# Kernel optimization log

Measured on AMD Instinct MI355X. Metric: run time of the kernel, lower is better.

Reference implementation:

```python
import jax, jax.numpy as jnp
import numpy as np

B, D, R = 4096, 1024, 256
DT = 0.01
DT_SCALE = 1.0

# Yoshida 4th-order coefficients
_W1 = 1.0 / (2.0 - 2.0 ** (1.0 / 3.0))
_W0 = -(2.0 ** (1.0 / 3.0)) / (2.0 - 2.0 ** (1.0 / 3.0))
C1 = _W1 / 2.0
C2 = (_W0 + _W1) / 2.0
C3 = C2
C4 = C1
D1 = _W1
D2 = _W0
D3 = _W1


def setup_inputs() -> dict:
    key = jax.random.key(0)
    k1, k2, k3, k4, k5 = jax.random.split(key, 5)
    x = jax.random.normal(k1, (B, D), dtype=jnp.float32)
    v = jax.random.normal(k2, (B, D), dtype=jnp.float32)
    force = jax.random.normal(k3, (B, D), dtype=jnp.float32)
    # low-rank christoffel factors, scaled for numerical stability
    U = jax.random.normal(k4, (R, D), dtype=jnp.float32) * (1.0 / np.sqrt(D))
    W = jax.random.normal(k5, (D, R), dtype=jnp.float32) * (1.0 / np.sqrt(R))
    return {"x": x, "v": v, "force": force, "U": U, "W": W}


def _christoffel(tv, tx, U, W):
    # Gamma(v) = W @ (U v)^2  (low-rank quadratic form; x unused, matching
    # the gfn yoshida_fused(U, W) signature)
    h = jnp.einsum("rd,bd->br", U, tv)  # [B, R]
    return jnp.einsum("dr,br->bd", W, h * h)  # [B, D]


def reference(x, v, force, U, W):
    dt = DT * DT_SCALE

    def acceleration(tx, tv):
        return -_christoffel(tv, tx, U, W) + force

    x1 = x + C1 * dt * v
    v1 = v + D1 * dt * acceleration(x1, v)
    x2 = x1 + C2 * dt * v1
    v2 = v1 + D2 * dt * acceleration(x2, v1)
    x3 = x2 + C3 * dt * v2
    v3 = v2 + D3 * dt * acceleration(x3, v2)
    x_final = x3 + C4 * dt * v3
    return (x_final, v3)
```

## Files before the change

kernel.cpp:

```cpp
#include <hip/hip_runtime.h>


#define BSZ 4096
#define DD 1024
#define RR 256

#define U_OFF 0u
#define W_OFF (512u * 1024u)
#define M_OFF (1024u * 1024u)

typedef unsigned char uchar;
typedef unsigned int uint;
typedef unsigned short ushort;
typedef __attribute__((ext_vector_type(4))) float f32x4;
typedef __attribute__((ext_vector_type(4))) uint uint4v;
typedef __attribute__((ext_vector_type(8))) short short8;

__device__ inline uint f2bf1(float x) {
    uint u = __builtin_bit_cast(uint, x);
    return (u + 0x7FFFu + ((u >> 16) & 1u)) >> 16;
}
__device__ inline uint f2bf2(float lo, float hi) {
    return f2bf1(lo) | (f2bf1(hi) << 16);
}
__device__ inline uint cvt2(float a, float b) {
    const __bf16 lo = (__bf16)a, hi = (__bf16)b;
    return (uint)__builtin_bit_cast(ushort, lo) |
           ((uint)__builtin_bit_cast(ushort, hi) << 16);
}
__device__ inline uint4v frag8(const float4 a, const float4 b) {
    uint4v o;
    o.x = cvt2(a.x, a.y); o.y = cvt2(a.z, a.w);
    o.z = cvt2(b.x, b.y); o.w = cvt2(b.z, b.w);
    return o;
}

__global__ __launch_bounds__(256) void prep_kernel(
    const float* __restrict__ U, const float* __restrict__ W,
    uchar* __restrict__ ws)
{
    if (blockIdx.x < 192) {
        const int g = blockIdx.x * 256 + threadIdx.x;
        const int l = g & 63;
        const float* src;
        size_t dst;
        if (g < 32768) {
            const int slice = g >> 6, nt = slice >> 5, p = slice & 31;
            src = U + (size_t)(nt * 16 + (l & 15)) * DD + p * 32 + (l >> 4) * 8;
            dst = U_OFF + (size_t)slice * 1024 + l * 16;
        } else {
            const int g2 = g - 32768;
            const int slice = g2 >> 6, dt_ = slice >> 3, p = slice & 7;
            src = W + (size_t)(dt_ * 16 + (l & 15)) * RR + p * 32 + (l >> 4) * 8;
            dst = W_OFF + (size_t)slice * 1024 + l * 16;
        }
        const float4 a0 = *reinterpret_cast<const float4*>(src);
        const float4 a1 = *reinterpret_cast<const float4*>(src + 4);
        uint4v o;
        o.x = f2bf2(a0.x, a0.y); o.y = f2bf2(a0.z, a0.w);
        o.z = f2bf2(a1.x, a1.y); o.w = f2bf2(a1.z, a1.w);
        *reinterpret_cast<uint4v*>(ws + dst) = o;
    } else {
        const int bid = blockIdx.x - 192;
        const int rt = bid >> 4, ct = bid & 15;
        const int r = rt * 16 + (threadIdx.x >> 4);
        const int c = ct * 16 + (threadIdx.x & 15);
        const float* ur = U + (size_t)r * DD;
        const float* wc = W + c;
        float acc[8];
        #pragma unroll
        for (int i = 0; i < 8; ++i) acc[i] = 0.f;
        #pragma unroll 4
        for (int k = 0; k < DD; k += 8) {
            const float4 u0 = *reinterpret_cast<const float4*>(ur + k);
            const float4 u1 = *reinterpret_cast<const float4*>(ur + k + 4);
            acc[0] += u0.x * wc[(size_t)(k + 0) * RR];
            acc[1] += u0.y * wc[(size_t)(k + 1) * RR];
            acc[2] += u0.z * wc[(size_t)(k + 2) * RR];
            acc[3] += u0.w * wc[(size_t)(k + 3) * RR];
            acc[4] += u1.x * wc[(size_t)(k + 4) * RR];
            acc[5] += u1.y * wc[(size_t)(k + 5) * RR];
            acc[6] += u1.z * wc[(size_t)(k + 6) * RR];
            acc[7] += u1.w * wc[(size_t)(k + 7) * RR];
        }
        const float s = ((acc[0] + acc[1]) + (acc[2] + acc[3]))
                      + ((acc[4] + acc[5]) + (acc[6] + acc[7]));
        const int slice = ((r >> 4) << 3) + (c >> 5);
        const int ll = (r & 15) | (((c >> 3) & 3) << 4);
        *reinterpret_cast<ushort*>(
            ws + M_OFF + (size_t)slice * 1024 + ll * 16 + (c & 7) * 2)
            = (ushort)f2bf1(s);
    }
}

__global__ __launch_bounds__(1024) void yoshida_fused_kernel(
    const float* __restrict__ x_in,
    const float* __restrict__ v_in,
    const float* __restrict__ force,
    const uchar* __restrict__ ws,
    float* __restrict__ x_out,
    float* __restrict__ v_out)
{
    __shared__ __align__(16) uchar vA[32768];
    __shared__ __align__(16) uchar fA[32768];
    __shared__ __align__(16) uchar H2B0[8192];
    __shared__ __align__(16) uchar H2B1[8192];
    __shared__ __align__(16) uchar PB[8192];
    __shared__ __align__(16) uchar QB[8192];

    const int tid = threadIdx.x;
    const int w = tid >> 6, l = tid & 63;
    const int m = l & 15, q = l >> 4;
    const int b0 = blockIdx.x * 16;

    constexpr double CBRT2 = 1.2599210498948731647672106072782;
    constexpr double W1c = 1.0 / (2.0 - CBRT2);
    constexpr double W0c = -CBRT2 * W1c;
    constexpr double DTd = 0.01;
    constexpr double D1 = W1c, D2 = W0c, D3 = W1c;
    constexpr double C2c = (W0c + W1c) * 0.5, C4c = W1c * 0.5;
    constexpr double E1 = (C2c + C2c + C4c) * D1;
    constexpr double E2 = (C2c + C4c) * D2;
    constexpr double E3 = C4c * D3;
    const float dtf = (float)DTd, dt2 = (float)(DTd * DTd);
    const float se = (float)(E1 + E2 + E3);

    #pragma unroll
    for (int j = 0; j < 2; ++j) {
        const int p = 2 * w + j;
        const size_t so = (size_t)(b0 + m) * DD + p * 32 + q * 8;
        const float4 v0_ = *reinterpret_cast<const float4*>(v_in + so);
        const float4 v1_ = *reinterpret_cast<const float4*>(v_in + so + 4);
        const float4 f0_ = *reinterpret_cast<const float4*>(force + so);
        const float4 f1_ = *reinterpret_cast<const float4*>(force + so + 4);
        *reinterpret_cast<uint4v*>(vA + (size_t)p * 1024 + l * 16) = frag8(v0_, v1_);
        *reinterpret_cast<uint4v*>(fA + (size_t)p * 1024 + l * 16) = frag8(f0_, f1_);
    }

    const uchar* const up = ws + U_OFF + ((size_t)(w * 32) << 10) + l * 16;
    uint4v ub[8];
    #pragma unroll
    for (int p = 0; p < 8; ++p)
        ub[p] = *reinterpret_cast<const uint4v*>(up + ((size_t)p << 10));

    __syncthreads();

    f32x4 h = {0.f, 0.f, 0.f, 0.f}, g = {0.f, 0.f, 0.f, 0.f};
    #pragma unroll
    for (int p = 0; p < 32; ++p) {
        const uint4v uc = ub[p & 7];
        if (p < 24)
            ub[p & 7] = *reinterpret_cast<const uint4v*>(up + ((size_t)(p + 8) << 10));
        const short8 ua = __builtin_bit_cast(short8, uc);
        const short8 va = __builtin_bit_cast(short8,
            *reinterpret_cast<const uint4v*>(vA + ((size_t)p << 10) + l * 16));
        const short8 fa = __builtin_bit_cast(short8,
            *reinterpret_cast<const uint4v*>(fA + ((size_t)p << 10) + l * 16));
        h = __builtin_amdgcn_mfma_f32_16x16x32_bf16(ua, va, h, 0, 0, 0);
        g = __builtin_amdgcn_mfma_f32_16x16x32_bf16(ua, fa, g, 0, 0, 0);
    }

    const uchar* const mp = ws + M_OFF + ((size_t)(w * 8) << 10) + l * 16;
    uint4v mb[8];
    #pragma unroll
    for (int p = 0; p < 8; ++p)
        mb[p] = *reinterpret_cast<const uint4v*>(mp + ((size_t)p << 10));

    const int k0 = 16 * w + 4 * q;
    const int p0 = k0 >> 5;
    const int lp = ((k0 & 31) >> 3) * 16 + m;
    const int j0 = k0 & 7;
    const int hoff = p0 * 1024 + lp * 16 + j0 * 2;

    f32x4 P, Q;
    {
        float h2[4];
        #pragma unroll
        for (int i = 0; i < 4; ++i) h2[i] = h[i] * h[i];
        #pragma unroll
        for (int i = 0; i < 4; ++i) {
            P[i] = (float)D1 * h2[i];
            Q[i] = (float)E1 * h2[i];
        }
        *reinterpret_cast<uint*>(H2B0 + hoff)     = f2bf2(h2[0], h2[1]);
        *reinterpret_cast<uint*>(H2B0 + hoff + 4) = f2bf2(h2[2], h2[3]);
    }

    __syncthreads();
    {
        f32x4 acc = {0.f, 0.f, 0.f, 0.f};
        #pragma unroll
        for (int p = 0; p < 8; ++p) {
            const short8 hb = __builtin_bit_cast(short8,
                *reinterpret_cast<const uint4v*>(H2B0 + ((size_t)p << 10) + l * 16));
            acc = __builtin_amdgcn_mfma_f32_16x16x32_bf16(
                      __builtin_bit_cast(short8, mb[p]), hb, acc, 0, 0, 0);
        }
        const float cg = (float)(DTd * D1);
        #pragma unroll
        for (int i = 0; i < 4; ++i) h[i] += cg * (g[i] - acc[i]);
    }
    {
        float h2[4];
        #pragma unroll
        for (int i = 0; i < 4; ++i) h2[i] = h[i] * h[i];
        #pragma unroll
        for (int i = 0; i < 4; ++i) {
            P[i] += (float)D2 * h2[i];
            Q[i] += (float)E2 * h2[i];
        }
        *reinterpret_cast<uint*>(H2B1 + hoff)     = f2bf2(h2[0], h2[1]);
        *reinterpret_cast<uint*>(H2B1 + hoff + 4) = f2bf2(h2[2], h2[3]);
    }
    __syncthreads();
    {
        f32x4 acc = {0.f, 0.f, 0.f, 0.f};
        #pragma unroll
        for (int p = 0; p < 8; ++p) {
            const short8 hb = __builtin_bit_cast(short8,
                *reinterpret_cast<const uint4v*>(H2B1 + ((size_t)p << 10) + l * 16));
            acc = __builtin_amdgcn_mfma_f32_16x16x32_bf16(
                      __builtin_bit_cast(short8, mb[p]), hb, acc, 0, 0, 0);
        }
        const float cg = (float)(DTd * D2);
        #pragma unroll
        for (int i = 0; i < 4; ++i) h[i] += cg * (g[i] - acc[i]);
    }
    {
        float h2[4];
        #pragma unroll
        for (int i = 0; i < 4; ++i) h2[i] = h[i] * h[i];
        #pragma unroll
        for (int i = 0; i < 4; ++i) {
            P[i] += (float)D3 * h2[i];
            Q[i] += (float)E3 * h2[i];
        }
    }
    *reinterpret_cast<uint*>(PB + hoff)     = f2bf2(P[0], P[1]);
    *reinterpret_cast<uint*>(PB + hoff + 4) = f2bf2(P[2], P[3]);
    *reinterpret_cast<uint*>(QB + hoff)     = f2bf2(Q[0], Q[1]);
    *reinterpret_cast<uint*>(QB + hoff + 4) = f2bf2(Q[2], Q[3]);

    const uchar* const wpb = ws + W_OFF + l * 16;
    uint4v wb[4][2];
    #pragma unroll
    for (int p = 0; p < 4; ++p) {
        wb[p][0] = *reinterpret_cast<const uint4v*>(wpb + (size_t)((4 * w)     * 8 + p) * 1024);
        wb[p][1] = *reinterpret_cast<const uint4v*>(wpb + (size_t)((4 * w + 1) * 8 + p) * 1024);
    }

    __syncthreads();

    #pragma unroll
    for (int half = 0; half < 2; ++half) {
        const int t0 = 4 * w + half * 2;
        f32x4 aV[2] = {{0.f,0.f,0.f,0.f}, {0.f,0.f,0.f,0.f}};
        f32x4 aX[2] = {{0.f,0.f,0.f,0.f}, {0.f,0.f,0.f,0.f}};
        #pragma unroll
        for (int p = 0; p < 8; ++p) {
            const uint4v c0 = wb[p & 3][0];
            const uint4v c1 = wb[p & 3][1];
            if (p < 4) {
                wb[p & 3][0] = *reinterpret_cast<const uint4v*>(
                    wpb + (size_t)((t0)     * 8 + p + 4) * 1024);
                wb[p & 3][1] = *reinterpret_cast<const uint4v*>(
                    wpb + (size_t)((t0 + 1) * 8 + p + 4) * 1024);
            } else if (half == 0) {
                wb[p & 3][0] = *reinterpret_cast<const uint4v*>(
                    wpb + (size_t)((t0 + 2) * 8 + (p - 4)) * 1024);
                wb[p & 3][1] = *reinterpret_cast<const uint4v*>(
                    wpb + (size_t)((t0 + 3) * 8 + (p - 4)) * 1024);
            }
            const short8 pb = __builtin_bit_cast(short8,
                *reinterpret_cast<const uint4v*>(PB + ((size_t)p << 10) + l * 16));
            const short8 qb = __builtin_bit_cast(short8,
                *reinterpret_cast<const uint4v*>(QB + ((size_t)p << 10) + l * 16));
            const short8 w0 = __builtin_bit_cast(short8, c0);
            const short8 w1 = __builtin_bit_cast(short8, c1);
            aV[0] = __builtin_amdgcn_mfma_f32_16x16x32_bf16(w0, pb, aV[0], 0, 0, 0);
            aV[1] = __builtin_amdgcn_mfma_f32_16x16x32_bf16(w1, pb, aV[1], 0, 0, 0);
            aX[0] = __builtin_amdgcn_mfma_f32_16x16x32_bf16(w0, qb, aX[0], 0, 0, 0);
            aX[1] = __builtin_amdgcn_mfma_f32_16x16x32_bf16(w1, qb, aX[1], 0, 0, 0);
        }
        #pragma unroll
        for (int t = 0; t < 2; ++t) {
            const size_t gib = (size_t)(b0 + m) * DD + (t0 + t) * 16 + 4 * q;
            const float4 fv = *reinterpret_cast<const float4*>(force + gib);
            const float4 v0 = *reinterpret_cast<const float4*>(v_in + gib);
            const float4 x0 = *reinterpret_cast<const float4*>(x_in + gib);
            float4 vo, xo;
            vo.x = v0.x + dtf * fv.x - dtf * aV[t][0];
            vo.y = v0.y + dtf * fv.y - dtf * aV[t][1];
            vo.z = v0.z + dtf * fv.z - dtf * aV[t][2];
            vo.w = v0.w + dtf * fv.w - dtf * aV[t][3];
            xo.x = x0.x + dtf * v0.x + dt2 * se * fv.x - dt2 * aX[t][0];
            xo.y = x0.y + dtf * v0.y + dt2 * se * fv.y - dt2 * aX[t][1];
            xo.z = x0.z + dtf * v0.z + dt2 * se * fv.z - dt2 * aX[t][2];
            xo.w = x0.w + dtf * v0.w + dt2 * se * fv.w - dt2 * aX[t][3];
            *reinterpret_cast<float4*>(v_out + gib) = vo;
            *reinterpret_cast<float4*>(x_out + gib) = xo;
        }
    }
}

extern "C" void kernel_launch(void* const* d_in, const int* in_sizes, int n_in,
                              void* d_out, int out_size, void* d_ws, size_t ws_size,
                              hipStream_t stream) {
    const float* x     = (const float*)d_in[0];
    const float* v     = (const float*)d_in[1];
    const float* force = (const float*)d_in[2];
    const float* U     = (const float*)d_in[3];
    const float* W     = (const float*)d_in[4];

    float* x_out = (float*)d_out;
    float* v_out = x_out + (size_t)BSZ * DD;

    uchar* ws = (uchar*)d_ws;

    prep_kernel<<<dim3(448), dim3(256), 0, stream>>>(U, W, ws);
    yoshida_fused_kernel<<<dim3(BSZ / 16), dim3(1024), 0, stream>>>(
        x, v, force, ws, x_out, v_out);
}
```

Measured before the change: 148.0 us.

## Split fused integrator into H/G projection kernel and D-split iteration kernel

Breaks the single fused kernel into a separate kernel that computes the U projections of v and force, storing them as fp32 in workspace, and an iteration kernel launched with twice as many blocks, each covering half of D for the output GEMM. The UW product is now computed with MFMA in its own kernel instead of scalar FMAs. The aim is more parallelism and less serial work per block. The cost is two extra launches and an HBM round-trip for the H/G intermediates, and the redundant Christoffel iterations now run in both halves.

```diff
diff --git a/kernel.cpp b/kernel.cpp
--- a/kernel.cpp
+++ b/kernel.cpp
@@ -8,6 +8,8 @@
 #define U_OFF 0u
 #define W_OFF (512u * 1024u)
 #define M_OFF (1024u * 1024u)
+#define H_OFF (2u * 1024u * 1024u)
+#define G_OFF (6u * 1024u * 1024u)
 
 typedef unsigned char uchar;
 typedef unsigned int uint;
@@ -35,74 +37,142 @@
     return o;
 }
 
-__global__ __launch_bounds__(256) void prep_kernel(
+__global__ __launch_bounds__(256) void pack_kernel(
     const float* __restrict__ U, const float* __restrict__ W,
     uchar* __restrict__ ws)
 {
-    if (blockIdx.x < 192) {
-        const int g = blockIdx.x * 256 + threadIdx.x;
-        const int l = g & 63;
-        const float* src;
-        size_t dst;
-        if (g < 32768) {
-            const int slice = g >> 6, nt = slice >> 5, p = slice & 31;
-            src = U + (size_t)(nt * 16 + (l & 15)) * DD + p * 32 + (l >> 4) * 8;
-            dst = U_OFF + (size_t)slice * 1024 + l * 16;
-        } else {
-            const int g2 = g - 32768;
-            const int slice = g2 >> 6, dt_ = slice >> 3, p = slice & 7;
-            src = W + (size_t)(dt_ * 16 + (l & 15)) * RR + p * 32 + (l >> 4) * 8;
-            dst = W_OFF + (size_t)slice * 1024 + l * 16;
-        }
-        const float4 a0 = *reinterpret_cast<const float4*>(src);
-        const float4 a1 = *reinterpret_cast<const float4*>(src + 4);
-        uint4v o;
-        o.x = f2bf2(a0.x, a0.y); o.y = f2bf2(a0.z, a0.w);
-        o.z = f2bf2(a1.x, a1.y); o.w = f2bf2(a1.z, a1.w);
-        *reinterpret_cast<uint4v*>(ws + dst) = o;
+    const int g = blockIdx.x * 256 + threadIdx.x;
+    const int l = g & 63;
+    const float* src;
+    size_t dst;
+    if (g < 32768) {
+        const int slice = g >> 6, nt = slice >> 5, p = slice & 31;
+        src = U + (size_t)(nt * 16 + (l & 15)) * DD + p * 32 + (l >> 4) * 8;
+        dst = U_OFF + (size_t)slice * 1024 + l * 16;
     } else {
-        const int bid = blockIdx.x - 192;
-        const int rt = bid >> 4, ct = bid & 15;
-        const int r = rt * 16 + (threadIdx.x >> 4);
-        const int c = ct * 16 + (threadIdx.x & 15);
-        const float* ur = U + (size_t)r * DD;
-        const float* wc = W + c;
-        float acc[8];
-        #pragma unroll
-        for (int i = 0; i < 8; ++i) acc[i] = 0.f;
-        #pragma unroll 4
-        for (int k = 0; k < DD; k += 8) {
-            const float4 u0 = *reinterpret_cast<const float4*>(ur + k);
-            const float4 u1 = *reinterpret_cast<const float4*>(ur + k + 4);
-            acc[0] += u0.x * wc[(size_t)(k + 0) * RR];
-            acc[1] += u0.y * wc[(size_t)(k + 1) * RR];
-            acc[2] += u0.z * wc[(size_t)(k + 2) * RR];
-            acc[3] += u0.w * wc[(size_t)(k + 3) * RR];
-            acc[4] += u1.x * wc[(size_t)(k + 4) * RR];
-            acc[5] += u1.y * wc[(size_t)(k + 5) * RR];
-            acc[6] += u1.z * wc[(size_t)(k + 6) * RR];
-            acc[7] += u1.w * wc[(size_t)(k + 7) * RR];
-        }
-        const float s = ((acc[0] + acc[1]) + (acc[2] + acc[3]))
-                      + ((acc[4] + acc[5]) + (acc[6] + acc[7]));
+        const int g2 = g - 32768;
+        const int slice = g2 >> 6, dt_ = slice >> 3, p = slice & 7;
+        src = W + (size_t)(dt_ * 16 + (l & 15)) * RR + p * 32 + (l >> 4) * 8;
+        dst = W_OFF + (size_t)slice * 1024 + l * 16;
+    }
+    const float4 a0 = *reinterpret_cast<const float4*>(src);
+    const float4 a1 = *reinterpret_cast<const float4*>(src + 4);
+    uint4v o;
+    o.x = f2bf2(a0.x, a0.y); o.y = f2bf2(a0.z, a0.w);
+    o.z = f2bf2(a1.x, a1.y); o.w = f2bf2(a1.z, a1.w);
+    *reinterpret_cast<uint4v*>(ws + dst) = o;
+}
+
+__global__ __launch_bounds__(256) void mm_kernel(
+    const float* __restrict__ W, uchar* __restrict__ ws)
+{
+    const int tid = threadIdx.x;
+    const int wv = tid >> 6, l = tid & 63;
+    const int m_ = l & 15, q = l >> 4;
+    const int task = blockIdx.x * 4 + wv;
+    const int rt = task >> 4, ct = task & 15;
+
+    const uchar* ua_base = ws + U_OFF + ((size_t)(rt * 32) << 10) + l * 16;
+    const float* wc = W + ct * 16 + m_;
+
+    f32x4 acc = {0.f, 0.f, 0.f, 0.f};
+    #pragma unroll 8
+    for (int p = 0; p < 32; ++p) {
+        const uint4v ua = *reinterpret_cast<const uint4v*>(ua_base + ((size_t)p << 10));
+        const int dbase = p * 32 + q * 8;
+        float w8[8];
+        #pragma unroll
+        for (int j = 0; j < 8; ++j) w8[j] = wc[(size_t)(dbase + j) * RR];
+        uint4v bb;
+        bb.x = cvt2(w8[0], w8[1]); bb.y = cvt2(w8[2], w8[3]);
+        bb.z = cvt2(w8[4], w8[5]); bb.w = cvt2(w8[6], w8[7]);
+        acc = __builtin_amdgcn_mfma_f32_16x16x32_bf16(
+                  __builtin_bit_cast(short8, ua),
+                  __builtin_bit_cast(short8, bb), acc, 0, 0, 0);
+    }
+    #pragma unroll
+    for (int i = 0; i < 4; ++i) {
+        const int r = rt * 16 + 4 * q + i;
+        const int c = ct * 16 + m_;
         const int slice = ((r >> 4) << 3) + (c >> 5);
         const int ll = (r & 15) | (((c >> 3) & 3) << 4);
         *reinterpret_cast<ushort*>(
             ws + M_OFF + (size_t)slice * 1024 + ll * 16 + (c & 7) * 2)
-            = (ushort)f2bf1(s);
-    }
-}
-
-__global__ __launch_bounds__(1024) void yoshida_fused_kernel(
+            = (ushort)f2bf1(acc[i]);
+    }
+}
+
+__global__ __launch_bounds__(512) void hg_kernel(
+    const float* __restrict__ v_in, const float* __restrict__ force,
+    const uchar* __restrict__ ws, float* __restrict__ Hf, float* __restrict__ Gf)
+{
+    __shared__ __align__(16) uchar vA[32768];
+    __shared__ __align__(16) uchar fA[32768];
+
+    const int tid = threadIdx.x;
+    const int w = tid >> 6, l = tid & 63;
+    const int m = l & 15, q = l >> 4;
+    const int b0 = blockIdx.x * 16;
+
+    #pragma unroll
+    for (int j = 0; j < 4; ++j) {
+        const int p = 4 * w + j;
+        const size_t so = (size_t)(b0 + m) * DD + p * 32 + q * 8;
+        const float4 v0 = *reinterpret_cast<const float4*>(v_in + so);
+        const float4 v1 = *reinterpret_cast<const float4*>(v_in + so + 4);
+        const float4 f0 = *reinterpret_cast<const float4*>(force + so);
+        const float4 f1 = *reinterpret_cast<const float4*>(force + so + 4);
+        *reinterpret_cast<uint4v*>(vA + (size_t)p * 1024 + l * 16) = frag8(v0, v1);
+        *reinterpret_cast<uint4v*>(fA + (size_t)p * 1024 + l * 16) = frag8(f0, f1);
+    }
+
+    const uchar* const upA = ws + U_OFF + ((size_t)(64 * w) << 10) + l * 16;
+    const uchar* const upB = upA + (32u << 10);
+    uint4v ubA[4], ubB[4];
+    #pragma unroll
+    for (int p = 0; p < 4; ++p) {
+        ubA[p] = *reinterpret_cast<const uint4v*>(upA + ((size_t)p << 10));
+        ubB[p] = *reinterpret_cast<const uint4v*>(upB + ((size_t)p << 10));
+    }
+
+    __syncthreads();
+
+    f32x4 hA = {0.f,0.f,0.f,0.f}, gA = {0.f,0.f,0.f,0.f};
+    f32x4 hB = {0.f,0.f,0.f,0.f}, gB = {0.f,0.f,0.f,0.f};
+    #pragma unroll
+    for (int p = 0; p < 32; ++p) {
+        const uint4v ucA = ubA[p & 3];
+        const uint4v ucB = ubB[p & 3];
+        if (p < 28) {
+            ubA[p & 3] = *reinterpret_cast<const uint4v*>(upA + ((size_t)(p + 4) << 10));
+            ubB[p & 3] = *reinterpret_cast<const uint4v*>(upB + ((size_t)(p + 4) << 10));
+        }
+        const short8 va = __builtin_bit_cast(short8,
+            *reinterpret_cast<const uint4v*>(vA + ((size_t)p << 10) + l * 16));
+        const short8 fa = __builtin_bit_cast(short8,
+            *reinterpret_cast<const uint4v*>(fA + ((size_t)p << 10) + l * 16));
+        hA = __builtin_amdgcn_mfma_f32_16x16x32_bf16(__builtin_bit_cast(short8, ucA), va, hA, 0, 0, 0);
+        gA = __builtin_amdgcn_mfma_f32_16x16x32_bf16(__builtin_bit_cast(short8, ucA), fa, gA, 0, 0, 0);
+        hB = __builtin_amdgcn_mfma_f32_16x16x32_bf16(__builtin_bit_cast(short8, ucB), va, hB, 0, 0, 0);
+        gB = __builtin_amdgcn_mfma_f32_16x16x32_bf16(__builtin_bit_cast(short8, ucB), fa, gB, 0, 0, 0);
+    }
+
+    const int k0A = 32 * w + 4 * q;
+    const size_t ho = (size_t)(b0 + m) * RR;
+    *reinterpret_cast<f32x4*>(Hf + ho + k0A)      = hA;
+    *reinterpret_cast<f32x4*>(Hf + ho + k0A + 16) = hB;
+    *reinterpret_cast<f32x4*>(Gf + ho + k0A)      = gA;
+    *reinterpret_cast<f32x4*>(Gf + ho + k0A + 16) = gB;
+}
+
+__global__ __launch_bounds__(1024) void iter_kernel(
     const float* __restrict__ x_in,
     const float* __restrict__ v_in,
     const float* __restrict__ force,
     const uchar* __restrict__ ws,
-    float* __restrict__ x_out,
-    float* __restrict__ v_out)
+    const float* __restrict__ Hf, const float* __restrict__ Gf,
+    float* __restrict__ x_out, float* __restrict__ v_out)
 {
-    __shared__ __align__(16) uchar vA[32768];
-    __shared__ __align__(16) uchar fA[32768];
     __shared__ __align__(16) uchar H2B0[8192];
     __shared__ __align__(16) uchar H2B1[8192];
     __shared__ __align__(16) uchar PB[8192];
@@ -111,7 +181,8 @@
     const int tid = threadIdx.x;
     const int w = tid >> 6, l = tid & 63;
     const int m = l & 15, q = l >> 4;
-    const int b0 = blockIdx.x * 16;
+    const int bt = blockIdx.x >> 1, dh = blockIdx.x & 1;
+    const int b0 = bt * 16;
 
     constexpr double CBRT2 = 1.2599210498948731647672106072782;
     constexpr double W1c = 1.0 / (2.0 - CBRT2);
@@ -125,48 +196,11 @@
     const float dtf = (float)DTd, dt2 = (float)(DTd * DTd);
     const float se = (float)(E1 + E2 + E3);
 
-    #pragma unroll
-    for (int j = 0; j < 2; ++j) {
-        const int p = 2 * w + j;
-        const size_t so = (size_t)(b0 + m) * DD + p * 32 + q * 8;
-        const float4 v0_ = *reinterpret_cast<const float4*>(v_in + so);
-        const float4 v1_ = *reinterpret_cast<const float4*>(v_in + so + 4);
-        const float4 f0_ = *reinterpret_cast<const float4*>(force + so);
-        const float4 f1_ = *reinterpret_cast<const float4*>(force + so + 4);
-        *reinterpret_cast<uint4v*>(vA + (size_t)p * 1024 + l * 16) = frag8(v0_, v1_);
-        *reinterpret_cast<uint4v*>(fA + (size_t)p * 1024 + l * 16) = frag8(f0_, f1_);
-    }
-
-    const uchar* const up = ws + U_OFF + ((size_t)(w * 32) << 10) + l * 16;
-    uint4v ub[8];
-    #pragma unroll
-    for (int p = 0; p < 8; ++p)
-        ub[p] = *reinterpret_cast<const uint4v*>(up + ((size_t)p << 10));
-
-    __syncthreads();
-
-    f32x4 h = {0.f, 0.f, 0.f, 0.f}, g = {0.f, 0.f, 0.f, 0.f};
-    #pragma unroll
-    for (int p = 0; p < 32; ++p) {
-        const uint4v uc = ub[p & 7];
-        if (p < 24)
-            ub[p & 7] = *reinterpret_cast<const uint4v*>(up + ((size_t)(p + 8) << 10));
-        const short8 ua = __builtin_bit_cast(short8, uc);
-        const short8 va = __builtin_bit_cast(short8,
-            *reinterpret_cast<const uint4v*>(vA + ((size_t)p << 10) + l * 16));
-        const short8 fa = __builtin_bit_cast(short8,
-            *reinterpret_cast<const uint4v*>(fA + ((size_t)p << 10) + l * 16));
-        h = __builtin_amdgcn_mfma_f32_16x16x32_bf16(ua, va, h, 0, 0, 0);
-        g = __builtin_amdgcn_mfma_f32_16x16x32_bf16(ua, fa, g, 0, 0, 0);
-    }
-
-    const uchar* const mp = ws + M_OFF + ((size_t)(w * 8) << 10) + l * 16;
-    uint4v mb[8];
-    #pragma unroll
-    for (int p = 0; p < 8; ++p)
-        mb[p] = *reinterpret_cast<const uint4v*>(mp + ((size_t)p << 10));
-
     const int k0 = 16 * w + 4 * q;
+    const size_t ho = (size_t)(b0 + m) * RR + k0;
+    f32x4 h = *reinterpret_cast<const f32x4*>(Hf + ho);
+    const f32x4 g = *reinterpret_cast<const f32x4*>(Gf + ho);
+
     const int p0 = k0 >> 5;
     const int lp = ((k0 & 31) >> 3) * 16 + m;
     const int j0 = k0 & 7;
@@ -185,6 +219,12 @@
         *reinterpret_cast<uint*>(H2B0 + hoff)     = f2bf2(h2[0], h2[1]);
         *reinterpret_cast<uint*>(H2B0 + hoff + 4) = f2bf2(h2[2], h2[3]);
     }
+
+    const uchar* const mp = ws + M_OFF + ((size_t)(w * 8) << 10) + l * 16;
+    uint4v mb[8];
+    #pragma unroll
+    for (int p = 0; p < 8; ++p)
+        mb[p] = *reinterpret_cast<const uint4v*>(mp + ((size_t)p << 10));
 
     __syncthreads();
     {
@@ -241,65 +281,57 @@
     *reinterpret_cast<uint*>(QB + hoff)     = f2bf2(Q[0], Q[1]);
     *reinterpret_cast<uint*>(QB + hoff + 4) = f2bf2(Q[2], Q[3]);
 
+    const int t0 = dh * 32 + 2 * w;
     const uchar* const wpb = ws + W_OFF + l * 16;
     uint4v wb[4][2];
     #pragma unroll
     for (int p = 0; p < 4; ++p) {
-        wb[p][0] = *reinterpret_cast<const uint4v*>(wpb + (size_t)((4 * w)     * 8 + p) * 1024);
-        wb[p][1] = *reinterpret_cast<const uint4v*>(wpb + (size_t)((4 * w + 1) * 8 + p) * 1024);
+        wb[p][0] = *reinterpret_cast<const uint4v*>(wpb + (size_t)((t0)     * 8 + p) * 1024);
+        wb[p][1] = *reinterpret_cast<const uint4v*>(wpb + (size_t)((t0 + 1) * 8 + p) * 1024);
     }
 
     __syncthreads();
 
-    #pragma unroll
-    for (int half = 0; half < 2; ++half) {
-        const int t0 = 4 * w + half * 2;
-        f32x4 aV[2] = {{0.f,0.f,0.f,0.f}, {0.f,0.f,0.f,0.f}};
-        f32x4 aX[2] = {{0.f,0.f,0.f,0.f}, {0.f,0.f,0.f,0.f}};
-        #pragma unroll
-        for (int p = 0; p < 8; ++p) {
-            const uint4v c0 = wb[p & 3][0];
-            const uint4v c1 = wb[p & 3][1];
-            if (p < 4) {
-                wb[p & 3][0] = *reinterpret_cast<const uint4v*>(
-                    wpb + (size_t)((t0)     * 8 + p + 4) * 1024);
-                wb[p & 3][1] = *reinterpret_cast<const uint4v*>(
-                    wpb + (size_t)((t0 + 1) * 8 + p + 4) * 1024);
-            } else if (half == 0) {
-                wb[p & 3][0] = *reinterpret_cast<const uint4v*>(
-                    wpb + (size_t)((t0 + 2) * 8 + (p - 4)) * 1024);
-                wb[p & 3][1] = *reinterpret_cast<const uint4v*>(
-                    wpb + (size_t)((t0 + 3) * 8 + (p - 4)) * 1024);
-            }
-            const short8 pb = __builtin_bit_cast(short8,
-                *reinterpret_cast<const uint4v*>(PB + ((size_t)p << 10) + l * 16));
-            const short8 qb = __builtin_bit_cast(short8,
-                *reinterpret_cast<const uint4v*>(QB + ((size_t)p << 10) + l * 16));
-            const short8 w0 = __builtin_bit_cast(short8, c0);
-            const short8 w1 = __builtin_bit_cast(short8, c1);
-            aV[0] = __builtin_amdgcn_mfma_f32_16x16x32_bf16(w0, pb, aV[0], 0, 0, 0);
-            aV[1] = __builtin_amdgcn_mfma_f32_16x16x32_bf16(w1, pb, aV[1], 0, 0, 0);
-            aX[0] = __builtin_amdgcn_mfma_f32_16x16x32_bf16(w0, qb, aX[0], 0, 0, 0);
-            aX[1] = __builtin_amdgcn_mfma_f32_16x16x32_bf16(w1, qb, aX[1], 0, 0, 0);
-        }
-        #pragma unroll
-        for (int t = 0; t < 2; ++t) {
-            const size_t gib = (size_t)(b0 + m) * DD + (t0 + t) * 16 + 4 * q;
-            const float4 fv = *reinterpret_cast<const float4*>(force + gib);
-            const float4 v0 = *reinterpret_cast<const float4*>(v_in + gib);
-            const float4 x0 = *reinterpret_cast<const float4*>(x_in + gib);
-            float4 vo, xo;
-            vo.x = v0.x + dtf * fv.x - dtf * aV[t][0];
-            vo.y = v0.y + dtf * fv.y - dtf * aV[t][1];
-            vo.z = v0.z + dtf * fv.z - dtf * aV[t][2];
-            vo.w = v0.w + dtf * fv.w - dtf * aV[t][3];
-            xo.x = x0.x + dtf * v0.x + dt2 * se * fv.x - dt2 * aX[t][0];
-            xo.y = x0.y + dtf * v0.y + dt2 * se * fv.y - dt2 * aX[t][1];
-            xo.z = x0.z + dtf * v0.z + dt2 * se * fv.z - dt2 * aX[t][2];
-            xo.w = x0.w + dtf * v0.w + dt2 * se * fv.w - dt2 * aX[t][3];
-            *reinterpret_cast<float4*>(v_out + gib) = vo;
-            *reinterpret_cast<float4*>(x_out + gib) = xo;
-        }
+    f32x4 aV[2] = {{0.f,0.f,0.f,0.f}, {0.f,0.f,0.f,0.f}};
+    f32x4 aX[2] = {{0.f,0.f,0.f,0.f}, {0.f,0.f,0.f,0.f}};
+    #pragma unroll
+    for (int p = 0; p < 8; ++p) {
+        const uint4v c0 = wb[p & 3][0];
+        const uint4v c1 = wb[p & 3][1];
+        if (p < 4) {
+            wb[p & 3][0] = *reinterpret_cast<const uint4v*>(
+                wpb + (size_t)((t0)     * 8 + p + 4) * 1024);
+            wb[p & 3][1] = *reinterpret_cast<const uint4v*>(
+                wpb + (size_t)((t0 + 1) * 8 + p + 4) * 1024);
+        }
+        const short8 pb = __builtin_bit_cast(short8,
+            *reinterpret_cast<const uint4v*>(PB + ((size_t)p << 10) + l * 16));
+        const short8 qb = __builtin_bit_cast(short8,
+            *reinterpret_cast<const uint4v*>(QB + ((size_t)p << 10) + l * 16));
+        const short8 w0 = __builtin_bit_cast(short8, c0);
+        const short8 w1 = __builtin_bit_cast(short8, c1);
+        aV[0] = __builtin_amdgcn_mfma_f32_16x16x32_bf16(w0, pb, aV[0], 0, 0, 0);
+        aV[1] = __builtin_amdgcn_mfma_f32_16x16x32_bf16(w1, pb, aV[1], 0, 0, 0);
+        aX[0] = __builtin_amdgcn_mfma_f32_16x16x32_bf16(w0, qb, aX[0], 0, 0, 0);
+        aX[1] = __builtin_amdgcn_mfma_f32_16x16x32_bf16(w1, qb, aX[1], 0, 0, 0);
+    }
+    #pragma unroll
+    for (int t = 0; t < 2; ++t) {
+        const size_t gib = (size_t)(b0 + m) * DD + (t0 + t) * 16 + 4 * q;
+        const float4 fv = *reinterpret_cast<const float4*>(force + gib);
+        const float4 v0 = *reinterpret_cast<const float4*>(v_in + gib);
+        const float4 x0 = *reinterpret_cast<const float4*>(x_in + gib);
+        float4 vo, xo;
+        vo.x = v0.x + dtf * fv.x - dtf * aV[t][0];
+        vo.y = v0.y + dtf * fv.y - dtf * aV[t][1];
+        vo.z = v0.z + dtf * fv.z - dtf * aV[t][2];
+        vo.w = v0.w + dtf * fv.w - dtf * aV[t][3];
+        xo.x = x0.x + dtf * v0.x + dt2 * se * fv.x - dt2 * aX[t][0];
+        xo.y = x0.y + dtf * v0.y + dt2 * se * fv.y - dt2 * aX[t][1];
+        xo.z = x0.z + dtf * v0.z + dt2 * se * fv.z - dt2 * aX[t][2];
+        xo.w = x0.w + dtf * v0.w + dt2 * se * fv.w - dt2 * aX[t][3];
+        *reinterpret_cast<float4*>(v_out + gib) = vo;
+        *reinterpret_cast<float4*>(x_out + gib) = xo;
     }
 }
 
@@ -316,8 +348,12 @@
     float* v_out = x_out + (size_t)BSZ * DD;
 
     uchar* ws = (uchar*)d_ws;
-
-    prep_kernel<<<dim3(448), dim3(256), 0, stream>>>(U, W, ws);
-    yoshida_fused_kernel<<<dim3(BSZ / 16), dim3(1024), 0, stream>>>(
-        x, v, force, ws, x_out, v_out);
-}
+    float* Hf = (float*)(ws + H_OFF);
+    float* Gf = (float*)(ws + G_OFF);
+
+    pack_kernel<<<dim3(192), dim3(256), 0, stream>>>(U, W, ws);
+    mm_kernel<<<dim3(64), dim3(256), 0, stream>>>(W, ws);
+    hg_kernel<<<dim3(BSZ / 16), dim3(512), 0, stream>>>(v, force, ws, Hf, Gf);
+    iter_kernel<<<dim3(2 * BSZ / 16), dim3(1024), 0, stream>>>(
+        x, v, force, ws, Hf, Gf, x_out, v_out);
+}
```

Result: faster. 139.7 us (-5.6%).
